# Kernel tuning notes

Measured on AMD Instinct MI355X. Metric: run time of the kernel, lower is better.

The kernel has to match this reference:

```python
import jax, jax.numpy as jnp
import numpy as np

EMBED = 1024
HEADS = 16
DIM_HEAD = EMBED // HEADS
N, L = 4, 2048


def setup_inputs() -> dict:
    key = jax.random.key(0)
    ks = jax.random.split(key, 12)
    s = 0.02
    return {
        "q": jax.random.normal(ks[0], (N, L, EMBED), jnp.float32),
        "k": jax.random.normal(ks[1], (N, L, EMBED), jnp.float32),
        "v": jax.random.normal(ks[2], (N, L, EMBED), jnp.float32),
        "padding_mask": jnp.ones((N, L), dtype=bool),
        "sequence_mask": jnp.zeros((L, L), dtype=bool),
        # Linear(in, out): store weight as [out, in] like torch, bias [out]
        "Wq": jax.random.normal(ks[3], (EMBED, EMBED), jnp.float32) * s,
        "bq": jnp.zeros((EMBED,), jnp.float32),
        "Wk": jax.random.normal(ks[4], (EMBED, EMBED), jnp.float32) * s,
        "bk": jnp.zeros((EMBED,), jnp.float32),
        "Wv": jax.random.normal(ks[5], (EMBED, EMBED), jnp.float32) * s,
        "bv": jnp.zeros((EMBED,), jnp.float32),
        "Wo": jax.random.normal(ks[6], (EMBED, EMBED), jnp.float32) * s,
        "bo": jnp.zeros((EMBED,), jnp.float32),
    }


def reference(q, k, v, padding_mask, sequence_mask, Wq, bq, Wk, bk, Wv, bv, Wo, bo):
    n, lq, _ = q.shape
    lk = k.shape[1]
    # input projections
    qp = (q @ Wq.T + bq).reshape(n, lq, HEADS, DIM_HEAD)
    kp = (k @ Wk.T + bk).reshape(n, lk, HEADS, DIM_HEAD)
    vp = (v @ Wv.T + bv).reshape(n, lk, HEADS, DIM_HEAD)
    # energy: [n, h, lq, lk]
    energy = jnp.einsum('nqhd,nkhd->nhqk', qp, kp)
    attention = jax.nn.softmax(energy / jnp.sqrt(jnp.float32(EMBED)), axis=3)
    # NOTE: the original torch code calls masked_fill (non in-place) and
    # discards the result, so padding_mask / sequence_mask have NO effect.
    # Dropout is also never applied in forward. Replicated faithfully.
    out = jnp.einsum('nhqk,nkhd->nqhd', attention, vp)
    out = out.reshape(n, lq, EMBED)
    return out @ Wo.T + bo
```

## Files before the change

kernel.cpp:

```cpp
#include <hip/hip_runtime.h>

typedef _Float16 f16;
typedef _Float16 f16x8 __attribute__((ext_vector_type(8)));
typedef _Float16 f16x4 __attribute__((ext_vector_type(4)));
typedef float f32x4 __attribute__((ext_vector_type(4)));

__device__ __forceinline__ f32x4 mfma16(f16x8 a, f16x8 b, f32x4 c) {
    return __builtin_amdgcn_mfma_f32_16x16x32_f16(a, b, c, 0, 0, 0);
}

template <typename T>
__device__ __forceinline__ void stage128(f16* dst, const T* src, int tid) {
#pragma unroll
    for (int i = 0; i < 4; ++i) {
        int id = tid + i * 256;
        int row = id >> 3, c = id & 7;
        const T* p = src + row * 1024 + c * 8;
        f16x8 h;
        if constexpr (sizeof(T) == 4) {
            f32x4 f0 = *(const f32x4*)p;
            f32x4 f1 = *(const f32x4*)(p + 4);
            h[0] = (f16)f0[0]; h[1] = (f16)f0[1]; h[2] = (f16)f0[2]; h[3] = (f16)f0[3];
            h[4] = (f16)f1[0]; h[5] = (f16)f1[1]; h[6] = (f16)f1[2]; h[7] = (f16)f1[3];
        } else {
            h = *(const f16x8*)p;
        }
        *(f16x8*)&dst[row * 64 + ((c ^ (row & 7)) << 3)] = h;
    }
}

template <typename TA, typename TB, bool OUT16, bool BIASROW>
__global__ __launch_bounds__(256, 2) void gemm128(const TA* __restrict__ A,
                                                  const TB* __restrict__ B,
                                                  const float* __restrict__ bias,
                                                  void* __restrict__ Cout, int ldo) {
    __shared__ __align__(16) f16 As[128 * 64];
    __shared__ __align__(16) f16 Bs[128 * 64];
    int tid = threadIdx.x;
    int lane = tid & 63, w = tid >> 6;
    int wm = w & 1, wn = w >> 1;
    int l15 = lane & 15, quad = lane >> 4;
    long m0 = (long)blockIdx.x * 128;
    long n0 = (long)blockIdx.y * 128;

    f32x4 acc[4][4] = {};

    for (int k0 = 0; k0 < 1024; k0 += 64) {
        __syncthreads();
        stage128<TA>(As, A + m0 * 1024 + k0, tid);
        stage128<TB>(Bs, B + n0 * 1024 + k0, tid);
        __syncthreads();
#pragma unroll
        for (int ks = 0; ks < 2; ++ks) {
            int cc = (ks * 4 + quad) ^ (l15 & 7);
            f16x8 af[4], bf[4];
#pragma unroll
            for (int t = 0; t < 4; ++t) {
                af[t] = *(const f16x8*)&As[(wm * 64 + t * 16 + l15) * 64 + cc * 8];
                bf[t] = *(const f16x8*)&Bs[(wn * 64 + t * 16 + l15) * 64 + cc * 8];
            }
#pragma unroll
            for (int i = 0; i < 4; ++i)
#pragma unroll
                for (int j = 0; j < 4; ++j)
                    acc[i][j] = mfma16(af[i], bf[j], acc[i][j]);
        }
    }

#pragma unroll
    for (int i = 0; i < 4; ++i) {
        int mrow = wm * 64 + i * 16 + quad * 4;
#pragma unroll
        for (int j = 0; j < 4; ++j) {
            int ncol = wn * 64 + j * 16 + l15;
            long gn = n0 + ncol;
#pragma unroll
            for (int r = 0; r < 4; ++r) {
                long gm = m0 + mrow + r;
                float v = acc[i][j][r] + (BIASROW ? bias[gm] : bias[gn]);
                if constexpr (OUT16)
                    ((f16*)Cout)[gm * ldo + gn] = (f16)v;
                else
                    ((float*)Cout)[gm * ldo + gn] = v;
            }
        }
    }
}

__global__ __launch_bounds__(256, 2) void attn128(const f16* __restrict__ Qp,
                                                  const f16* __restrict__ Kp,
                                                  const f16* __restrict__ Vt,
                                                  f16* __restrict__ Op) {
    __shared__ __align__(16) f16 Qs[128 * 64];
    __shared__ __align__(16) f16 Ks[64 * 64];
    __shared__ __align__(16) f16 Vs[64 * 64];
    __shared__ __align__(16) f16 Ps[128 * 64];
    __shared__ float lsi[128];

    int tid = threadIdx.x;
    int lane = tid & 63, w = tid >> 6;
    int l15 = lane & 15, quad = lane >> 4;
    int qt = blockIdx.x;
    int nh = blockIdx.y;
    int nb = nh >> 4, h = nh & 15;
    long tok0 = (long)nb * 2048;

    {
        const f16* src = Qp + (tok0 + qt * 128) * 1024 + h * 64;
#pragma unroll
        for (int i = 0; i < 4; ++i) {
            int id = tid + i * 256;
            int row = id >> 3, c = id & 7;
            f16x8 hv = *(const f16x8*)&src[row * 1024 + c * 8];
            *(f16x8*)&Qs[row * 64 + ((c ^ (row & 7)) << 3)] = hv;
        }
    }

    f32x4 oacc[2][4] = {};
    float rsum[2] = {0.f, 0.f};

    for (int kt = 0; kt < 32; ++kt) {
        __syncthreads();
        {
            const f16* ksrc = Kp + (tok0 + kt * 64) * 1024 + h * 64;
            const f16* vsrc = Vt + (long)(h * 64) * 8192 + tok0 + kt * 64;
#pragma unroll
            for (int i = 0; i < 2; ++i) {
                int id = tid + i * 256;
                int row = id >> 3, c = id & 7;
                f16x8 hv = *(const f16x8*)&ksrc[row * 1024 + c * 8];
                *(f16x8*)&Ks[row * 64 + ((c ^ (row & 7)) << 3)] = hv;
                f16x8 vv = *(const f16x8*)&vsrc[(long)row * 8192 + c * 8];
                *(f16x8*)&Vs[row * 64 + ((c ^ (row & 7)) << 3)] = vv;
            }
        }
        __syncthreads();

        f32x4 sacc[4][2] = {};
#pragma unroll
        for (int ks = 0; ks < 2; ++ks) {
            int cc = (ks * 4 + quad) ^ (l15 & 7);
            f16x8 af[4], bf[2];
#pragma unroll
            for (int t = 0; t < 4; ++t)
                af[t] = *(const f16x8*)&Ks[(t * 16 + l15) * 64 + cc * 8];
#pragma unroll
            for (int j = 0; j < 2; ++j)
                bf[j] = *(const f16x8*)&Qs[(w * 32 + j * 16 + l15) * 64 + cc * 8];
#pragma unroll
            for (int i = 0; i < 4; ++i)
#pragma unroll
                for (int j = 0; j < 2; ++j)
                    sacc[i][j] = mfma16(af[i], bf[j], sacc[i][j]);
        }

#pragma unroll
        for (int i = 0; i < 4; ++i) {
#pragma unroll
            for (int j = 0; j < 2; ++j) {
                f16x4 ph;
                float s = 0.f;
#pragma unroll
                for (int r = 0; r < 4; ++r) {
                    float p = __expf(sacc[i][j][r] * 0.03125f);
                    s += p;
                    ph[r] = (f16)p;
                }
                rsum[j] += s;
                int q = w * 32 + j * 16 + l15;
                int kl = i * 16 + quad * 4;
                int c = kl >> 3;
                *(f16x4*)&Ps[q * 64 + ((c ^ (q & 7)) << 3) + (kl & 7)] = ph;
            }
        }
        __syncthreads();

#pragma unroll
        for (int ks = 0; ks < 2; ++ks) {
            int cc = (ks * 4 + quad) ^ (l15 & 7);
            f16x8 af[2], bf[4];
#pragma unroll
            for (int i = 0; i < 2; ++i)
                af[i] = *(const f16x8*)&Ps[(w * 32 + i * 16 + l15) * 64 + cc * 8];
#pragma unroll
            for (int j = 0; j < 4; ++j)
                bf[j] = *(const f16x8*)&Vs[(j * 16 + l15) * 64 + cc * 8];
#pragma unroll
            for (int i = 0; i < 2; ++i)
#pragma unroll
                for (int j = 0; j < 4; ++j)
                    oacc[i][j] = mfma16(af[i], bf[j], oacc[i][j]);
        }
    }

#pragma unroll
    for (int j = 0; j < 2; ++j) {
        rsum[j] += __shfl_xor(rsum[j], 16, 64);
        rsum[j] += __shfl_xor(rsum[j], 32, 64);
    }
    if (lane < 16) {
        lsi[w * 32 + lane] = 1.0f / rsum[0];
        lsi[w * 32 + 16 + lane] = 1.0f / rsum[1];
    }
    __syncthreads();

    long otok = tok0 + (long)qt * 128;
#pragma unroll
    for (int i = 0; i < 2; ++i) {
        int qrow = w * 32 + i * 16 + quad * 4;
#pragma unroll
        for (int j = 0; j < 4; ++j) {
            int d = j * 16 + l15;
#pragma unroll
            for (int r = 0; r < 4; ++r) {
                float v = oacc[i][j][r] * lsi[qrow + r];
                Op[(otok + qrow + r) * 1024 + h * 64 + d] = (f16)v;
            }
        }
    }
}

__global__ void cvt_weights(const float* __restrict__ a, const float* __restrict__ b,
                            const float* __restrict__ c, const float* __restrict__ d,
                            f16* __restrict__ out) {
    int id = blockIdx.x * 256 + threadIdx.x;
    int m = id >> 18;
    const float* s = (m == 0) ? a : (m == 1) ? b : (m == 2) ? c : d;
    long off = (long)(id & 262143) * 4;
    f32x4 v = *(const f32x4*)(s + off);
    f16x4 h;
    h[0] = (f16)v[0]; h[1] = (f16)v[1]; h[2] = (f16)v[2]; h[3] = (f16)v[3];
    *(f16x4*)&out[(long)m * 1048576 + off] = h;
}

extern "C" void kernel_launch(void* const* d_in, const int* in_sizes, int n_in,
                              void* d_out, int out_size, void* d_ws, size_t ws_size,
                              hipStream_t stream) {
    const float* q  = (const float*)d_in[0];
    const float* k  = (const float*)d_in[1];
    const float* v  = (const float*)d_in[2];
    const float* Wq = (const float*)d_in[5];
    const float* bq = (const float*)d_in[6];
    const float* Wk = (const float*)d_in[7];
    const float* bk = (const float*)d_in[8];
    const float* Wv = (const float*)d_in[9];
    const float* bv = (const float*)d_in[10];
    const float* Wo = (const float*)d_in[11];
    const float* bo = (const float*)d_in[12];

    char* ws = (char*)d_ws;
    f16* wh = (f16*)ws;
    f16* Qp = (f16*)(ws + (8L << 20));
    f16* Kp = (f16*)(ws + (24L << 20));
    f16* Vt = (f16*)(ws + (40L << 20));
    f16* Op = (f16*)(ws + (56L << 20));

    cvt_weights<<<4096, 256, 0, stream>>>(Wq, Wk, Wv, Wo, wh);

    gemm128<float, f16, true, false><<<dim3(64, 8), 256, 0, stream>>>(q, wh, bq, Qp, 1024);
    gemm128<float, f16, true, false><<<dim3(64, 8), 256, 0, stream>>>(k, wh + 1048576, bk, Kp, 1024);
    gemm128<f16, float, true, true><<<dim3(8, 64), 256, 0, stream>>>(wh + 2097152, v, bv, Vt, 8192);

    attn128<<<dim3(16, 64), 256, 0, stream>>>(Qp, Kp, Vt, Op);

    gemm128<f16, f16, false, false><<<dim3(64, 8), 256, 0, stream>>>(Op, wh + 3145728, bo, (float*)d_out, 1024);
}
```

Baseline: 387.1 us.

## Pre-cast activations to fp16, stage tiles via direct global-to-LDS loads, double-buffer attention

All fp32 activations and weights are converted to fp16 in one kernel up front, so the GEMMs can read fp16 only. Both GEMM and attention stage tiles with global_load_lds, writing straight into LDS with the existing XOR swizzle folded into the source addresses, instead of going through registers. Attention double-buffers K/V tiles so the next tile's load overlaps the softmax and PV work, keeps Q fragments in registers, remaps blocks so heads are grouped per XCD, and packs probabilities with cvt_pkrtz. Workspace buffers are aliased to fit, which adds an extra full pass over the activations and relies on barriers to cover the asynchronous LDS loads.

```diff
diff --git a/kernel.cpp b/kernel.cpp
--- a/kernel.cpp
+++ b/kernel.cpp
@@ -1,54 +1,61 @@
 #include <hip/hip_runtime.h>
+#include <stdint.h>
 
 typedef _Float16 f16;
 typedef _Float16 f16x8 __attribute__((ext_vector_type(8)));
 typedef _Float16 f16x4 __attribute__((ext_vector_type(4)));
+typedef _Float16 f16x2 __attribute__((ext_vector_type(2)));
+typedef __fp16 h16x2 __attribute__((ext_vector_type(2)));
 typedef float f32x4 __attribute__((ext_vector_type(4)));
 
 __device__ __forceinline__ f32x4 mfma16(f16x8 a, f16x8 b, f32x4 c) {
     return __builtin_amdgcn_mfma_f32_16x16x32_f16(a, b, c, 0, 0, 0);
 }
 
-template <typename T>
-__device__ __forceinline__ void stage128(f16* dst, const T* src, int tid) {
-#pragma unroll
-    for (int i = 0; i < 4; ++i) {
-        int id = tid + i * 256;
-        int row = id >> 3, c = id & 7;
-        const T* p = src + row * 1024 + c * 8;
-        f16x8 h;
-        if constexpr (sizeof(T) == 4) {
-            f32x4 f0 = *(const f32x4*)p;
-            f32x4 f1 = *(const f32x4*)(p + 4);
-            h[0] = (f16)f0[0]; h[1] = (f16)f0[1]; h[2] = (f16)f0[2]; h[3] = (f16)f0[3];
-            h[4] = (f16)f1[0]; h[5] = (f16)f1[1]; h[6] = (f16)f1[2]; h[7] = (f16)f1[3];
-        } else {
-            h = *(const f16x8*)p;
-        }
-        *(f16x8*)&dst[row * 64 + ((c ^ (row & 7)) << 3)] = h;
-    }
-}
-
-template <typename TA, typename TB, bool OUT16, bool BIASROW>
-__global__ __launch_bounds__(256, 2) void gemm128(const TA* __restrict__ A,
-                                                  const TB* __restrict__ B,
-                                                  const float* __restrict__ bias,
-                                                  void* __restrict__ Cout, int ldo) {
+__device__ __forceinline__ void gload16(const f16* g, f16* l) {
+    __builtin_amdgcn_global_load_lds(
+        (const __attribute__((address_space(1))) uint32_t*)g,
+        (__attribute__((address_space(3))) uint32_t*)l, 16, 0, 0);
+}
+
+template <bool OUT16, bool BIASROW, bool XN>
+__global__ __launch_bounds__(256, 2) void gemm128h(const f16* __restrict__ A,
+                                                   const f16* __restrict__ B,
+                                                   const float* __restrict__ bias,
+                                                   void* __restrict__ Cout, long ldo) {
     __shared__ __align__(16) f16 As[128 * 64];
     __shared__ __align__(16) f16 Bs[128 * 64];
     int tid = threadIdx.x;
     int lane = tid & 63, w = tid >> 6;
     int wm = w & 1, wn = w >> 1;
     int l15 = lane & 15, quad = lane >> 4;
-    long m0 = (long)blockIdx.x * 128;
-    long n0 = (long)blockIdx.y * 128;
+    long m0 = (long)(XN ? blockIdx.y : blockIdx.x) * 128;
+    long n0 = (long)(XN ? blockIdx.x : blockIdx.y) * 128;
+
+    int rg = lane >> 3;
+    int cg = (lane & 7) ^ rg;
+    const f16* ag[4];
+    const f16* bg[4];
+    f16* al[4];
+    f16* bl[4];
+#pragma unroll
+    for (int t = 0; t < 4; ++t) {
+        int rb = (w * 4 + t) * 8;
+        ag[t] = A + (m0 + rb + rg) * 1024 + cg * 8;
+        bg[t] = B + (n0 + rb + rg) * 1024 + cg * 8;
+        al[t] = &As[rb * 64];
+        bl[t] = &Bs[rb * 64];
+    }
 
     f32x4 acc[4][4] = {};
 
     for (int k0 = 0; k0 < 1024; k0 += 64) {
         __syncthreads();
-        stage128<TA>(As, A + m0 * 1024 + k0, tid);
-        stage128<TB>(Bs, B + n0 * 1024 + k0, tid);
+#pragma unroll
+        for (int t = 0; t < 4; ++t) {
+            gload16(ag[t] + k0, al[t]);
+            gload16(bg[t] + k0, bl[t]);
+        }
         __syncthreads();
 #pragma unroll
         for (int ks = 0; ks < 2; ++ks) {
@@ -92,89 +99,96 @@
                                                   const f16* __restrict__ Vt,
                                                   f16* __restrict__ Op) {
     __shared__ __align__(16) f16 Qs[128 * 64];
-    __shared__ __align__(16) f16 Ks[64 * 64];
-    __shared__ __align__(16) f16 Vs[64 * 64];
+    __shared__ __align__(16) f16 Ks[2][64 * 64];
+    __shared__ __align__(16) f16 Vs[2][64 * 64];
     __shared__ __align__(16) f16 Ps[128 * 64];
     __shared__ float lsi[128];
 
     int tid = threadIdx.x;
     int lane = tid & 63, w = tid >> 6;
     int l15 = lane & 15, quad = lane >> 4;
-    int qt = blockIdx.x;
-    int nh = blockIdx.y;
+    int b = blockIdx.x;
+    int xcd = b & 7, slot = b >> 3;
+    int nh = xcd * 8 + (slot >> 4);
+    int qt = slot & 15;
     int nb = nh >> 4, h = nh & 15;
     long tok0 = (long)nb * 2048;
 
-    {
-        const f16* src = Qp + (tok0 + qt * 128) * 1024 + h * 64;
-#pragma unroll
-        for (int i = 0; i < 4; ++i) {
-            int id = tid + i * 256;
-            int row = id >> 3, c = id & 7;
-            f16x8 hv = *(const f16x8*)&src[row * 1024 + c * 8];
-            *(f16x8*)&Qs[row * 64 + ((c ^ (row & 7)) << 3)] = hv;
-        }
+    int rg = lane >> 3, cg = (lane & 7) ^ rg;
+
+    const f16* qsrc = Qp + (tok0 + qt * 128) * 1024 + h * 64;
+#pragma unroll
+    for (int t = 0; t < 4; ++t) {
+        int rb = w * 32 + t * 8;
+        gload16(qsrc + (rb + rg) * 1024 + cg * 8, &Qs[rb * 64]);
+    }
+    const f16* kbase = Kp + (tok0 + w * 16 + rg) * 1024 + h * 64 + cg * 8;
+    const f16* vbase = Vt + ((long)h * 64 + w * 16 + rg) * 8192 + tok0 + cg * 8;
+#pragma unroll
+    for (int t = 0; t < 2; ++t) {
+        gload16(kbase + t * 8 * 1024, &Ks[0][(w * 16 + t * 8) * 64]);
+        gload16(vbase + (long)t * 8 * 8192, &Vs[0][(w * 16 + t * 8) * 64]);
+    }
+    __syncthreads();
+
+    f16x8 qf[2][2];
+#pragma unroll
+    for (int ks = 0; ks < 2; ++ks) {
+        int cc = (ks * 4 + quad) ^ (l15 & 7);
+#pragma unroll
+        for (int j = 0; j < 2; ++j)
+            qf[ks][j] = *(const f16x8*)&Qs[(w * 32 + j * 16 + l15) * 64 + cc * 8];
     }
 
     f32x4 oacc[2][4] = {};
     float rsum[2] = {0.f, 0.f};
 
     for (int kt = 0; kt < 32; ++kt) {
-        __syncthreads();
-        {
-            const f16* ksrc = Kp + (tok0 + kt * 64) * 1024 + h * 64;
-            const f16* vsrc = Vt + (long)(h * 64) * 8192 + tok0 + kt * 64;
-#pragma unroll
-            for (int i = 0; i < 2; ++i) {
-                int id = tid + i * 256;
-                int row = id >> 3, c = id & 7;
-                f16x8 hv = *(const f16x8*)&ksrc[row * 1024 + c * 8];
-                *(f16x8*)&Ks[row * 64 + ((c ^ (row & 7)) << 3)] = hv;
-                f16x8 vv = *(const f16x8*)&vsrc[(long)row * 8192 + c * 8];
-                *(f16x8*)&Vs[row * 64 + ((c ^ (row & 7)) << 3)] = vv;
-            }
-        }
-        __syncthreads();
-
+        int cur = kt & 1;
         f32x4 sacc[4][2] = {};
 #pragma unroll
         for (int ks = 0; ks < 2; ++ks) {
             int cc = (ks * 4 + quad) ^ (l15 & 7);
-            f16x8 af[4], bf[2];
+            f16x8 af[4];
 #pragma unroll
             for (int t = 0; t < 4; ++t)
-                af[t] = *(const f16x8*)&Ks[(t * 16 + l15) * 64 + cc * 8];
-#pragma unroll
-            for (int j = 0; j < 2; ++j)
-                bf[j] = *(const f16x8*)&Qs[(w * 32 + j * 16 + l15) * 64 + cc * 8];
+                af[t] = *(const f16x8*)&Ks[cur][(t * 16 + l15) * 64 + cc * 8];
 #pragma unroll
             for (int i = 0; i < 4; ++i)
 #pragma unroll
                 for (int j = 0; j < 2; ++j)
-                    sacc[i][j] = mfma16(af[i], bf[j], sacc[i][j]);
-        }
-
+                    sacc[i][j] = mfma16(af[i], qf[ks][j], sacc[i][j]);
+        }
+        if (kt < 31) {
+            int nxt = cur ^ 1;
+            const f16* kp2 = kbase + (long)(kt + 1) * 65536;
+            const f16* vp2 = vbase + (kt + 1) * 64;
+#pragma unroll
+            for (int t = 0; t < 2; ++t) {
+                gload16(kp2 + t * 8 * 1024, &Ks[nxt][(w * 16 + t * 8) * 64]);
+                gload16(vp2 + (long)t * 8 * 8192, &Vs[nxt][(w * 16 + t * 8) * 64]);
+            }
+        }
 #pragma unroll
         for (int i = 0; i < 4; ++i) {
 #pragma unroll
             for (int j = 0; j < 2; ++j) {
+                float p0 = __expf(sacc[i][j][0] * 0.03125f);
+                float p1 = __expf(sacc[i][j][1] * 0.03125f);
+                float p2 = __expf(sacc[i][j][2] * 0.03125f);
+                float p3 = __expf(sacc[i][j][3] * 0.03125f);
+                rsum[j] += (p0 + p1) + (p2 + p3);
+                f16x2 lo = __builtin_bit_cast(f16x2, __builtin_amdgcn_cvt_pkrtz(p0, p1));
+                f16x2 hi = __builtin_bit_cast(f16x2, __builtin_amdgcn_cvt_pkrtz(p2, p3));
                 f16x4 ph;
-                float s = 0.f;
-#pragma unroll
-                for (int r = 0; r < 4; ++r) {
-                    float p = __expf(sacc[i][j][r] * 0.03125f);
-                    s += p;
-                    ph[r] = (f16)p;
-                }
-                rsum[j] += s;
-                int q = w * 32 + j * 16 + l15;
+                ph[0] = lo[0]; ph[1] = lo[1]; ph[2] = hi[0]; ph[3] = hi[1];
+                int qrow = w * 32 + j * 16 + l15;
                 int kl = i * 16 + quad * 4;
                 int c = kl >> 3;
-                *(f16x4*)&Ps[q * 64 + ((c ^ (q & 7)) << 3) + (kl & 7)] = ph;
+                *(f16x4*)&Ps[qrow * 64 + ((c ^ (qrow & 7)) << 3) + (kl & 7)] = ph;
             }
         }
         __syncthreads();
-
 #pragma unroll
         for (int ks = 0; ks < 2; ++ks) {
             int cc = (ks * 4 + quad) ^ (l15 & 7);
@@ -184,13 +198,14 @@
                 af[i] = *(const f16x8*)&Ps[(w * 32 + i * 16 + l15) * 64 + cc * 8];
 #pragma unroll
             for (int j = 0; j < 4; ++j)
-                bf[j] = *(const f16x8*)&Vs[(j * 16 + l15) * 64 + cc * 8];
+                bf[j] = *(const f16x8*)&Vs[cur][(j * 16 + l15) * 64 + cc * 8];
 #pragma unroll
             for (int i = 0; i < 2; ++i)
 #pragma unroll
                 for (int j = 0; j < 4; ++j)
                     oacc[i][j] = mfma16(af[i], bf[j], oacc[i][j]);
         }
+        __syncthreads();
     }
 
 #pragma unroll
@@ -220,17 +235,34 @@
     }
 }
 
-__global__ void cvt_weights(const float* __restrict__ a, const float* __restrict__ b,
-                            const float* __restrict__ c, const float* __restrict__ d,
-                            f16* __restrict__ out) {
-    int id = blockIdx.x * 256 + threadIdx.x;
-    int m = id >> 18;
-    const float* s = (m == 0) ? a : (m == 1) ? b : (m == 2) ? c : d;
-    long off = (long)(id & 262143) * 4;
-    f32x4 v = *(const f32x4*)(s + off);
-    f16x4 h;
-    h[0] = (f16)v[0]; h[1] = (f16)v[1]; h[2] = (f16)v[2]; h[3] = (f16)v[3];
-    *(f16x4*)&out[(long)m * 1048576 + off] = h;
+__global__ void cvt_all(const float* __restrict__ q, const float* __restrict__ k,
+                        const float* __restrict__ v, const float* __restrict__ w0,
+                        const float* __restrict__ w1, const float* __restrict__ w2,
+                        const float* __restrict__ w3, f16* __restrict__ qh,
+                        f16* __restrict__ kh, f16* __restrict__ vh,
+                        f16* __restrict__ wh) {
+    long id = (long)blockIdx.x * 256 + threadIdx.x;
+    const float* s;
+    f16* d;
+    long off;
+    if (id < 3145728) {
+        int which = (int)(id >> 20);
+        off = (id & 1048575) * 8;
+        s = which == 0 ? q : which == 1 ? k : v;
+        d = which == 0 ? qh : which == 1 ? kh : vh;
+    } else {
+        long id2 = id - 3145728;
+        int wi = (int)(id2 >> 17);
+        off = (id2 & 131071) * 8;
+        s = wi == 0 ? w0 : wi == 1 ? w1 : wi == 2 ? w2 : w3;
+        d = wh + (long)wi * 1048576;
+    }
+    f32x4 a = *(const f32x4*)(s + off);
+    f32x4 b = *(const f32x4*)(s + off + 4);
+    f16x8 hv;
+    hv[0] = (f16)a[0]; hv[1] = (f16)a[1]; hv[2] = (f16)a[2]; hv[3] = (f16)a[3];
+    hv[4] = (f16)b[0]; hv[5] = (f16)b[1]; hv[6] = (f16)b[2]; hv[7] = (f16)b[3];
+    *(f16x8*)(d + off) = hv;
 }
 
 extern "C" void kernel_launch(void* const* d_in, const int* in_sizes, int n_in,
@@ -249,19 +281,23 @@
     const float* bo = (const float*)d_in[12];
 
     char* ws = (char*)d_ws;
-    f16* wh = (f16*)ws;
-    f16* Qp = (f16*)(ws + (8L << 20));
-    f16* Kp = (f16*)(ws + (24L << 20));
-    f16* Vt = (f16*)(ws + (40L << 20));
-    f16* Op = (f16*)(ws + (56L << 20));
-
-    cvt_weights<<<4096, 256, 0, stream>>>(Wq, Wk, Wv, Wo, wh);
-
-    gemm128<float, f16, true, false><<<dim3(64, 8), 256, 0, stream>>>(q, wh, bq, Qp, 1024);
-    gemm128<float, f16, true, false><<<dim3(64, 8), 256, 0, stream>>>(k, wh + 1048576, bk, Kp, 1024);
-    gemm128<f16, float, true, true><<<dim3(8, 64), 256, 0, stream>>>(wh + 2097152, v, bv, Vt, 8192);
-
-    attn128<<<dim3(16, 64), 256, 0, stream>>>(Qp, Kp, Vt, Op);
-
-    gemm128<f16, f16, false, false><<<dim3(64, 8), 256, 0, stream>>>(Op, wh + 3145728, bo, (float*)d_out, 1024);
-}
+    f16* X  = (f16*)ws;
+    f16* Wh = (f16*)(ws + (16L << 20));
+    f16* Qp = (f16*)(ws + (24L << 20));
+    f16* Kp = (f16*)(ws + (40L << 20));
+    f16* Vt = (f16*)(ws + (56L << 20));
+    f16* qh = Kp;
+    f16* kh = Vt;
+    f16* vh = X;
+    f16* Op = X;
+
+    cvt_all<<<14336, 256, 0, stream>>>(q, k, v, Wq, Wk, Wv, Wo, qh, kh, vh, Wh);
+
+    gemm128h<true, false, false><<<dim3(64, 8), 256, 0, stream>>>(qh, Wh, bq, Qp, 1024);
+    gemm128h<true, false, false><<<dim3(64, 8), 256, 0, stream>>>(kh, Wh + 1048576, bk, Kp, 1024);
+    gemm128h<true, true, true><<<dim3(64, 8), 256, 0, stream>>>(Wh + 2097152, vh, bv, Vt, 8192);
+
+    attn128<<<1024, 256, 0, stream>>>(Qp, Kp, Vt, Op);
+
+    gemm128h<false, false, false><<<dim3(64, 8), 256, 0, stream>>>(Op, Wh + 3145728, bo, (float*)d_out, 1024);
+}
```

Result: faster. 343.2 us (-11.4%).
